# Kernel tuning notes

Measured on AMD Instinct MI355X. Metric: run time of the kernel, lower is better.

Reference implementation:

```python
import jax, jax.numpy as jnp
import numpy as np

B, S, D, H = 2, 2048, 1024, 16
HD = D // H  # head dim 64

def setup_inputs() -> dict:
    key = jax.random.key(0)
    k1, k2, k3 = jax.random.split(key, 3)
    x = jax.random.normal(k1, (B, S, D), dtype=jnp.float32)
    w_attn = jax.random.normal(k2, (D, 3 * D), dtype=jnp.float32) * (1.0 / np.sqrt(D))
    w_proj = jax.random.normal(k3, (D, D), dtype=jnp.float32) * (1.0 / np.sqrt(D))
    return {"x": x, "w_attn": w_attn, "w_proj": w_proj}

def reference(x, w_attn, w_proj):
    b, s, d = x.shape
    qkv = x @ w_attn                      # [b, s, 3d]
    q, k, v = jnp.split(qkv, 3, axis=-1)
    def heads(t):
        return t.reshape(b, s, H, HD).transpose(0, 2, 1, 3)  # [b, h, s, hd]
    q, k, v = heads(q), heads(k), heads(v)
    scale = 1.0 / np.sqrt(HD)
    att = jnp.einsum('bhqd,bhkd->bhqk', q, k) * scale        # [b, h, s, s]
    causal = jnp.tril(jnp.ones((s, s), dtype=bool))
    att = jnp.where(causal[None, None], att, -jnp.inf)
    att = jax.nn.softmax(att, axis=-1)
    y = jnp.einsum('bhqk,bhkd->bhqd', att, v)                # [b, h, s, hd]
    y = y.transpose(0, 2, 1, 3).reshape(b, s, d)
    return y @ w_proj
```

## Files before the change

### kernel.cpp

```cpp
#include <hip/hip_runtime.h>

#define B_  2
#define S_  2048
#define D_  1024
#define H_  16
#define HD_ 64
#define TD_ 3072

typedef __bf16 bf16x8 __attribute__((ext_vector_type(8)));
typedef float  f32x4  __attribute__((ext_vector_type(4)));
typedef float  f32x16 __attribute__((ext_vector_type(16)));

#define AS1 __attribute__((address_space(1)))
#define AS3 __attribute__((address_space(3)))

#define MASKVAL (-60000.0f)
#define MINITVAL (-30000.0f)

__device__ __forceinline__ unsigned short f2bf(float f) {
  return __builtin_bit_cast(unsigned short, (__bf16)f);
}

__device__ __forceinline__ unsigned int pkbf(float lo, float hi) {
  unsigned int r;
  asm("v_cvt_pk_bf16_f32 %0, %1, %2" : "=v"(r) : "v"(lo), "v"(hi));
  return r;
}

__device__ __forceinline__ void plswap(unsigned int& a, unsigned int& b) {
  asm volatile("v_permlane32_swap_b32 %0, %1" : "+v"(a), "+v"(b));
}

__device__ __forceinline__ float exp2a(float x) {
  return __builtin_amdgcn_exp2f(x);
}

__device__ __forceinline__ float xmax32(float x) {
  return fmaxf(x, __shfl_xor(x, 32, 64));
}
__device__ __forceinline__ float xadd32(float x) {
  return x + __shfl_xor(x, 32, 64);
}

__device__ __forceinline__ void gload16(const void* g, void* l) {
  __builtin_amdgcn_global_load_lds((const AS1 void*)g, (AS3 void*)l, 16, 0, 0);
}

__global__ __launch_bounds__(256) void k_convert_x(const float* __restrict__ x,
                                                   unsigned short* __restrict__ xb) {
  const int i = (blockIdx.x * 256 + threadIdx.x) * 4;
  float4 v = *(const float4*)(x + i);
  ushort4 o;
  o.x = f2bf(v.x); o.y = f2bf(v.y); o.z = f2bf(v.z); o.w = f2bf(v.w);
  *(ushort4*)(xb + i) = o;
}

__global__ __launch_bounds__(256) void k_prep_w(const float* __restrict__ wa,
                                                const float* __restrict__ wp,
                                                unsigned short* __restrict__ waT,
                                                unsigned short* __restrict__ wpT) {
  __shared__ __align__(16) unsigned short tile[64][72];
  const int t = threadIdx.x;
  const int bx = blockIdx.x;
  const float* w;
  unsigned short* wt;
  int C, c0;
  if (bx < 48) { w = wa; wt = waT; C = TD_; c0 = bx * 64; }
  else         { w = wp; wt = wpT; C = D_;  c0 = (bx - 48) * 64; }
  const int R = D_;
  const int r0 = blockIdx.y * 64;
  const int rr = t >> 2, cc = (t & 3) * 16;
  const float* src = w + (size_t)(r0 + rr) * C + c0 + cc;
#pragma unroll
  for (int j = 0; j < 16; j += 4) {
    float4 v = *(const float4*)(src + j);
    tile[rr][cc + j + 0] = f2bf(v.x);
    tile[rr][cc + j + 1] = f2bf(v.y);
    tile[rr][cc + j + 2] = f2bf(v.z);
    tile[rr][cc + j + 3] = f2bf(v.w);
  }
  __syncthreads();
  unsigned short* dst = wt + (size_t)(c0 + rr) * R + r0 + cc;
#pragma unroll
  for (int j = 0; j < 16; j += 2) {
    unsigned int pk = (unsigned int)tile[cc + j][rr] |
                      ((unsigned int)tile[cc + j + 1][rr] << 16);
    *(unsigned int*)(dst + j) = pk;
  }
}

__global__ __launch_bounds__(256) void k_gemm_qkv(const unsigned short* __restrict__ A,
                                                  const unsigned short* __restrict__ Bt,
                                                  unsigned short* __restrict__ qb,
                                                  unsigned short* __restrict__ kp,
                                                  unsigned short* __restrict__ vp) {
  __shared__ __align__(16) unsigned short ldsA[64 * 64];
  __shared__ __align__(16) unsigned short ldsB[128 * 64];
  const int K = D_;
  const int t = threadIdx.x;
  const int lane = t & 63;
  const int wid = t >> 6;
  const int wr = wid >> 1, wc = wid & 1;
  const int bx = blockIdx.x;
  const int bm = blockIdx.y * 64;
  const int bn = (((bx & 7) * 3) + (bx >> 3)) * 128;
  const int r = lane & 15, g = lane >> 4;

  f32x4 acc[2][4] = {};

  for (int kt = 0; kt < K; kt += 64) {
#pragma unroll
    for (int c = 0; c < 2; ++c) {
      const int idx = c * 256 + t;
      const int row = idx >> 3;
      const int col = ((idx & 7) ^ (row & 7)) * 8;
      gload16(A + (size_t)(bm + row) * K + kt + col, ldsA + idx * 8);
    }
#pragma unroll
    for (int c = 0; c < 4; ++c) {
      const int idx = c * 256 + t;
      const int row = idx >> 3;
      const int col = ((idx & 7) ^ (row & 7)) * 8;
      gload16(Bt + (size_t)(bn + row) * K + kt + col, ldsB + idx * 8);
    }
    asm volatile("s_waitcnt vmcnt(0)" ::: "memory");
    __syncthreads();
#pragma unroll
    for (int ks = 0; ks < 2; ++ks) {
      bf16x8 af[2], bfr[4];
#pragma unroll
      for (int m = 0; m < 2; ++m) {
        const int row = wr * 32 + m * 16 + r;
        const int slot = (ks * 4 + g) ^ (row & 7);
        af[m] = *(const bf16x8*)(ldsA + row * 64 + slot * 8);
      }
#pragma unroll
      for (int n = 0; n < 4; ++n) {
        const int row = wc * 64 + n * 16 + r;
        const int slot = (ks * 4 + g) ^ (row & 7);
        bfr[n] = *(const bf16x8*)(ldsB + row * 64 + slot * 8);
      }
#pragma unroll
      for (int m = 0; m < 2; ++m)
#pragma unroll
        for (int n = 0; n < 4; ++n)
          acc[m][n] = __builtin_amdgcn_mfma_f32_16x16x32_bf16(af[m], bfr[n],
                                                              acc[m][n], 0, 0, 0);
    }
    __syncthreads();
  }

  const int row0 = bm + wr * 32 + g * 4;
  const int col0 = bn + wc * 64 + r;
  const int region = bn >> 10;
  const int b = blockIdx.y >> 5;
  const int sbase = (bm & 2047) + wr * 32 + g * 4;

  if (region == 0) {
#pragma unroll
    for (int m = 0; m < 2; ++m)
#pragma unroll
      for (int n = 0; n < 4; ++n)
#pragma unroll
        for (int i = 0; i < 4; ++i)
          qb[(size_t)(row0 + m * 16 + i) * D_ + col0 + n * 16] = f2bf(acc[m][n][i]);
  } else if (region == 1) {
    const int h = ((bn - 1024) >> 6) + wc;
    unsigned short* kpb = kp + (size_t)(b * 16 + h) * 131072;
#pragma unroll
    for (int m = 0; m < 2; ++m) {
      const int s = sbase + m * 16;
      const int tau = s >> 5, l = s & 31;
#pragma unroll
      for (int n = 0; n < 4; ++n) {
        unsigned short* kq = kpb + tau * 2048 +
                             (n * 64 + (r >> 3) * 32 + l) * 8 + (r & 7);
        kq[0]  = f2bf(acc[m][n][0]);
        kq[8]  = f2bf(acc[m][n][1]);
        kq[16] = f2bf(acc[m][n][2]);
        kq[24] = f2bf(acc[m][n][3]);
      }
    }
  } else {
    const int h = ((bn - 2048) >> 6) + wc;
    unsigned short* vpb = vp + (size_t)(b * 16 + h) * 131072;
#pragma unroll
    for (int m = 0; m < 2; ++m) {
      const int s = sbase + m * 16;
      const int tau2 = s >> 6;
      const int T = (s >> 5) & 1, c16 = (s >> 4) & 1, hi8 = (s >> 3) & 1;
      const int u = s & 7;
#pragma unroll
      for (int n = 0; n < 4; ++n) {
        const int half = n >> 1;
        const int l = (n & 1) * 16 + r;
        const int tid = T * 256 + c16 * 128 + half * 64 + hi8 * 32 + l;
        unsigned long long pk2 =
            (unsigned long long)pkbf(acc[m][n][0], acc[m][n][1]) |
            ((unsigned long long)pkbf(acc[m][n][2], acc[m][n][3]) << 32);
        *(unsigned long long*)(vpb + tau2 * 4096 + tid * 8 + u) = pk2;
      }
    }
  }
}

__global__ __launch_bounds__(256) void k_gemm_bt64(const unsigned short* __restrict__ A,
                                                   const unsigned short* __restrict__ Bt,
                                                   float* __restrict__ C,
                                                   int Ndim, int K) {
  __shared__ __align__(16) unsigned short ldsA[64 * 64];
  __shared__ __align__(16) unsigned short ldsB[128 * 64];
  const int t = threadIdx.x;
  const int lane = t & 63;
  const int wid = t >> 6;
  const int wr = wid >> 1, wc = wid & 1;
  const int bm = blockIdx.y * 64, bn = blockIdx.x * 128;
  const int r = lane & 15, g = lane >> 4;

  f32x4 acc[2][4] = {};

  for (int kt = 0; kt < K; kt += 64) {
#pragma unroll
    for (int c = 0; c < 2; ++c) {
      const int idx = c * 256 + t;
      const int row = idx >> 3;
      const int col = ((idx & 7) ^ (row & 7)) * 8;
      gload16(A + (size_t)(bm + row) * K + kt + col, ldsA + idx * 8);
    }
#pragma unroll
    for (int c = 0; c < 4; ++c) {
      const int idx = c * 256 + t;
      const int row = idx >> 3;
      const int col = ((idx & 7) ^ (row & 7)) * 8;
      gload16(Bt + (size_t)(bn + row) * K + kt + col, ldsB + idx * 8);
    }
    asm volatile("s_waitcnt vmcnt(0)" ::: "memory");
    __syncthreads();
#pragma unroll
    for (int ks = 0; ks < 2; ++ks) {
      bf16x8 af[2], bfr[4];
#pragma unroll
      for (int m = 0; m < 2; ++m) {
        const int row = wr * 32 + m * 16 + r;
        const int slot = (ks * 4 + g) ^ (row & 7);
        af[m] = *(const bf16x8*)(ldsA + row * 64 + slot * 8);
      }
#pragma unroll
      for (int n = 0; n < 4; ++n) {
        const int row = wc * 64 + n * 16 + r;
        const int slot = (ks * 4 + g) ^ (row & 7);
        bfr[n] = *(const bf16x8*)(ldsB + row * 64 + slot * 8);
      }
#pragma unroll
      for (int m = 0; m < 2; ++m)
#pragma unroll
        for (int n = 0; n < 4; ++n)
          acc[m][n] = __builtin_amdgcn_mfma_f32_16x16x32_bf16(af[m], bfr[n],
                                                              acc[m][n], 0, 0, 0);
    }
    __syncthreads();
  }

  const int row0 = bm + wr * 32 + g * 4;
  const int col0 = bn + wc * 64 + r;
#pragma unroll
  for (int m = 0; m < 2; ++m)
#pragma unroll
    for (int n = 0; n < 4; ++n)
#pragma unroll
      for (int i = 0; i < 4; ++i)
        C[(size_t)(row0 + m * 16 + i) * Ndim + col0 + n * 16] = acc[m][n][i];
}

__global__ __launch_bounds__(256, 4) void k_attn(const unsigned short* __restrict__ qb,
                                                 const unsigned short* __restrict__ kp,
                                                 const unsigned short* __restrict__ vp,
                                                 unsigned short* __restrict__ y) {
  __shared__ __align__(16) float Om[2][64][32];
  __shared__ float Ml[2][2][32];
  const int t = threadIdx.x;
  const int lane = t & 63, w = t >> 6;
  const int l31 = lane & 31, hi = lane >> 5;
  const int pr = w & 1;
  const int parity = w >> 1;
  const int bh = blockIdx.x & 31;
  const int j = blockIdx.x >> 5;
  const int sj = pr ? (63 - j) : j;
  const int h = bh & 15, b = bh >> 4;
  const int qbase = 32 * sj;
  const int qq = qbase + l31;

  const float SC = 0.125f * 1.44269504f;

  bf16x8 qf[4];
  {
    const unsigned short* qp = qb + (size_t)(b * S_ + qbase + l31) * D_ + h * HD_;
#pragma unroll
    for (int c = 0; c < 4; ++c) {
      bf16x8 rl = *(const bf16x8*)(qp + c * 16 + hi * 8);
      union { unsigned int u[4]; bf16x8 v; } pl;
#pragma unroll
      for (int jx = 0; jx < 4; ++jx)
        pl.u[jx] = pkbf((float)rl[2 * jx] * SC, (float)rl[2 * jx + 1] * SC);
      qf[c] = pl.v;
    }
  }

  float mr = MINITVAL, lr = 0.f;
  f32x16 o0 = {}, o1 = {};

  const unsigned short* kpb = kp + (size_t)bh * 131072;
  const unsigned short* vpb = vp + (size_t)bh * 131072;

  const int tmax = (32 * sj + 31) >> 6;

  for (int kvt = parity; kvt <= tmax; kvt += 2) {
    const int kv0 = kvt << 6;
    bf16x8 kf[2][4];
#pragma unroll
    for (int T = 0; T < 2; ++T)
#pragma unroll
      for (int c = 0; c < 4; ++c)
        kf[T][c] = *(const bf16x8*)(kpb + (size_t)(kvt * 8 + T * 4 + c) * 512 +
                                    lane * 8);

    f32x16 s0 = {}, s1 = {};
    __builtin_amdgcn_s_setprio(1);
#pragma unroll
    for (int c = 0; c < 4; ++c) {
      s0 = __builtin_amdgcn_mfma_f32_32x32x16_bf16(kf[0][c], qf[c], s0, 0, 0, 0);
      s1 = __builtin_amdgcn_mfma_f32_32x32x16_bf16(kf[1][c], qf[c], s1, 0, 0, 0);
    }
    __builtin_amdgcn_s_setprio(0);

    float am[4] = {MASKVAL, MASKVAL, MASKVAL, MASKVAL};
    if (kv0 + 63 > qbase) {
#pragma unroll
      for (int rg = 0; rg < 16; ++rg) {
        const int kv = kv0 + (rg & 3) + 8 * (rg >> 2) + 4 * hi;
        float v0 = (kv <= qq) ? s0[rg] : MASKVAL; s0[rg] = v0;
        float v1 = (kv + 32 <= qq) ? s1[rg] : MASKVAL; s1[rg] = v1;
        am[rg & 3] = fmaxf(am[rg & 3], fmaxf(v0, v1));
      }
    } else {
#pragma unroll
      for (int rg = 0; rg < 16; ++rg)
        am[rg & 3] = fmaxf(am[rg & 3], fmaxf(s0[rg], s1[rg]));
    }
    const float pm = xmax32(fmaxf(fmaxf(am[0], am[1]), fmaxf(am[2], am[3])));

    const float nm = fmaxf(mr, pm);
    if (!__all(nm - mr <= 12.0f)) {
      const float cr = exp2a(mr - nm);
      mr = nm;
      lr *= cr;
#pragma unroll
      for (int rg = 0; rg < 16; ++rg) { o0[rg] *= cr; o1[rg] *= cr; }
    }

    float as[4] = {0.f, 0.f, 0.f, 0.f};
#pragma unroll
    for (int rg = 0; rg < 16; ++rg) {
      const float p0 = exp2a(s0[rg] - mr); s0[rg] = p0;
      const float p1 = exp2a(s1[rg] - mr); s1[rg] = p1;
      as[rg & 3] += p0 + p1;
    }
    lr += xadd32((as[0] + as[1]) + (as[2] + as[3]));

    const unsigned short* vpt = vpb + (size_t)kvt * 4096;
    __builtin_amdgcn_s_setprio(1);
#pragma unroll
    for (int T = 0; T < 2; ++T) {
      const f32x16& sT = T ? s1 : s0;
#pragma unroll
      for (int c = 0; c < 2; ++c) {
        unsigned int x0 = pkbf(sT[8 * c + 0], sT[8 * c + 1]);
        unsigned int x1 = pkbf(sT[8 * c + 2], sT[8 * c + 3]);
        unsigned int x2 = pkbf(sT[8 * c + 4], sT[8 * c + 5]);
        unsigned int x3 = pkbf(sT[8 * c + 6], sT[8 * c + 7]);
        plswap(x0, x2);
        plswap(x1, x3);
        union { unsigned int u[4]; bf16x8 v; } pb;
        pb.u[0] = x0; pb.u[1] = x1; pb.u[2] = x2; pb.u[3] = x3;
        const unsigned short* vb = vpt + (size_t)((T * 2 + c) * 2) * 512 + lane * 8;
        bf16x8 vf0 = *(const bf16x8*)(vb);
        bf16x8 vf1 = *(const bf16x8*)(vb + 512);
        o0 = __builtin_amdgcn_mfma_f32_32x32x16_bf16(vf0, pb.v, o0, 0, 0, 0);
        o1 = __builtin_amdgcn_mfma_f32_32x32x16_bf16(vf1, pb.v, o1, 0, 0, 0);
      }
    }
    __builtin_amdgcn_s_setprio(0);
  }

  __syncthreads();
  if (parity) {
#pragma unroll
    for (int tt = 0; tt < 2; ++tt) {
      const f32x16& o = tt ? o1 : o0;
#pragma unroll
      for (int rg = 0; rg < 16; ++rg) {
        const int row = tt * 32 + (rg & 3) + 8 * (rg >> 2) + 4 * hi;
        Om[pr][row][l31] = o[rg];
      }
    }
    if (!hi) {
      Ml[pr][0][l31] = mr;
      Ml[pr][1][l31] = lr;
    }
  }
  __syncthreads();
  if (!parity) {
    const float mo = Ml[pr][0][l31];
    const float lo2 = Ml[pr][1][l31];
    const float mm = fmaxf(mr, mo);
    const float ce = exp2a(mr - mm), co = exp2a(mo - mm);
    const float lt = lr * ce + lo2 * co;
    const float ic = ce / lt, io = co / lt;
    unsigned short* yp = y + (size_t)(b * S_ + qbase + l31) * D_ + h * HD_;
#pragma unroll
    for (int tt = 0; tt < 2; ++tt) {
      const f32x16& o = tt ? o1 : o0;
#pragma unroll
      for (int rg = 0; rg < 16; rg += 2) {
        const int row = tt * 32 + (rg & 3) + 8 * (rg >> 2) + 4 * hi;
        const float v0 = o[rg] * ic + Om[pr][row][l31] * io;
        const float v1 = o[rg + 1] * ic + Om[pr][row + 1][l31] * io;
        *(unsigned int*)(yp + row) = pkbf(v0, v1);
      }
    }
  }
}

extern "C" void kernel_launch(void* const* d_in, const int* in_sizes, int n_in,
                              void* d_out, int out_size, void* d_ws, size_t ws_size,
                              hipStream_t stream) {
  const float* x  = (const float*)d_in[0];
  const float* wa = (const float*)d_in[1];
  const float* wp = (const float*)d_in[2];
  float* out = (float*)d_out;

  char* ws = (char*)d_ws;
  unsigned short* xb  = (unsigned short*)(ws + 0);
  unsigned short* waT = (unsigned short*)(ws + 8388608);
  unsigned short* wpT = (unsigned short*)(ws + 14680064);
  unsigned short* qb  = (unsigned short*)(ws + 16777216);
  unsigned short* kp  = (unsigned short*)(ws + 25165824);
  unsigned short* vp  = (unsigned short*)(ws + 33554432);
  unsigned short* yb  = (unsigned short*)(ws + 41943040);

  k_convert_x<<<4096, 256, 0, stream>>>(x, xb);
  k_prep_w<<<dim3(64, 16), 256, 0, stream>>>(wa, wp, waT, wpT);
  k_gemm_qkv<<<dim3(24, 64), 256, 0, stream>>>(xb, waT, qb, kp, vp);
  k_attn<<<1024, 256, 0, stream>>>(qb, kp, vp, yb);
  k_gemm_bt64<<<dim3(8, 64), 256, 0, stream>>>(yb, wpT, out, D_, D_);
}
```

Baseline: 111.4 us.

## Double-buffer QKV GEMM LDS loads and merge input-prep kernels into one launch

The QKV GEMM now uses two LDS buffers, so the global-to-LDS loads for the next K tile are issued before the MFMAs run on the current tile. MFMA sections also get raised wave priority via s_setprio. Separately, the x conversion and weight transpose kernels are merged into one launch with a flattened grid, removing one kernel launch. Double buffering doubles LDS use per block (48KB), which may lower occupancy.

```diff
diff --git a/kernel.cpp b/kernel.cpp
--- a/kernel.cpp
+++ b/kernel.cpp
@@ -46,29 +46,33 @@
   __builtin_amdgcn_global_load_lds((const AS1 void*)g, (AS3 void*)l, 16, 0, 0);
 }
 
-__global__ __launch_bounds__(256) void k_convert_x(const float* __restrict__ x,
-                                                   unsigned short* __restrict__ xb) {
-  const int i = (blockIdx.x * 256 + threadIdx.x) * 4;
-  float4 v = *(const float4*)(x + i);
-  ushort4 o;
-  o.x = f2bf(v.x); o.y = f2bf(v.y); o.z = f2bf(v.z); o.w = f2bf(v.w);
-  *(ushort4*)(xb + i) = o;
-}
-
-__global__ __launch_bounds__(256) void k_prep_w(const float* __restrict__ wa,
-                                                const float* __restrict__ wp,
-                                                unsigned short* __restrict__ waT,
-                                                unsigned short* __restrict__ wpT) {
+__global__ __launch_bounds__(256) void k_prep(const float* __restrict__ x,
+                                              const float* __restrict__ wa,
+                                              const float* __restrict__ wp,
+                                              unsigned short* __restrict__ xb,
+                                              unsigned short* __restrict__ waT,
+                                              unsigned short* __restrict__ wpT) {
   __shared__ __align__(16) unsigned short tile[64][72];
   const int t = threadIdx.x;
-  const int bx = blockIdx.x;
+  const int bid = blockIdx.x;
+  if (bid < 4096) {
+    const int i = (bid * 256 + t) * 4;
+    float4 v = *(const float4*)(x + i);
+    ushort4 o;
+    o.x = f2bf(v.x); o.y = f2bf(v.y); o.z = f2bf(v.z); o.w = f2bf(v.w);
+    *(ushort4*)(xb + i) = o;
+    return;
+  }
+  const int idx = bid - 4096;
+  const int bx = idx & 63;
+  const int by = idx >> 6;
   const float* w;
   unsigned short* wt;
   int C, c0;
   if (bx < 48) { w = wa; wt = waT; C = TD_; c0 = bx * 64; }
   else         { w = wp; wt = wpT; C = D_;  c0 = (bx - 48) * 64; }
   const int R = D_;
-  const int r0 = blockIdx.y * 64;
+  const int r0 = by * 64;
   const int rr = t >> 2, cc = (t & 3) * 16;
   const float* src = w + (size_t)(r0 + rr) * C + c0 + cc;
 #pragma unroll
@@ -94,8 +98,8 @@
                                                   unsigned short* __restrict__ qb,
                                                   unsigned short* __restrict__ kp,
                                                   unsigned short* __restrict__ vp) {
-  __shared__ __align__(16) unsigned short ldsA[64 * 64];
-  __shared__ __align__(16) unsigned short ldsB[128 * 64];
+  __shared__ __align__(16) unsigned short ldsA[2][64 * 64];
+  __shared__ __align__(16) unsigned short ldsB[2][128 * 64];
   const int K = D_;
   const int t = threadIdx.x;
   const int lane = t & 63;
@@ -108,23 +112,32 @@
 
   f32x4 acc[2][4] = {};
 
-  for (int kt = 0; kt < K; kt += 64) {
+  auto stage = [&](int buf, int kt) {
 #pragma unroll
     for (int c = 0; c < 2; ++c) {
       const int idx = c * 256 + t;
       const int row = idx >> 3;
       const int col = ((idx & 7) ^ (row & 7)) * 8;
-      gload16(A + (size_t)(bm + row) * K + kt + col, ldsA + idx * 8);
+      gload16(A + (size_t)(bm + row) * K + kt + col, &ldsA[buf][idx * 8]);
     }
 #pragma unroll
     for (int c = 0; c < 4; ++c) {
       const int idx = c * 256 + t;
       const int row = idx >> 3;
       const int col = ((idx & 7) ^ (row & 7)) * 8;
-      gload16(Bt + (size_t)(bn + row) * K + kt + col, ldsB + idx * 8);
-    }
-    asm volatile("s_waitcnt vmcnt(0)" ::: "memory");
-    __syncthreads();
+      gload16(Bt + (size_t)(bn + row) * K + kt + col, &ldsB[buf][idx * 8]);
+    }
+  };
+
+  stage(0, 0);
+  asm volatile("s_waitcnt vmcnt(0)" ::: "memory");
+  __syncthreads();
+
+  int cur = 0;
+  for (int kt = 0; kt < K; kt += 64) {
+    if (kt + 64 < K) stage(cur ^ 1, kt + 64);
+
+    __builtin_amdgcn_s_setprio(1);
 #pragma unroll
     for (int ks = 0; ks < 2; ++ks) {
       bf16x8 af[2], bfr[4];
@@ -132,13 +145,13 @@
       for (int m = 0; m < 2; ++m) {
         const int row = wr * 32 + m * 16 + r;
         const int slot = (ks * 4 + g) ^ (row & 7);
-        af[m] = *(const bf16x8*)(ldsA + row * 64 + slot * 8);
+        af[m] = *(const bf16x8*)(&ldsA[cur][row * 64 + slot * 8]);
       }
 #pragma unroll
       for (int n = 0; n < 4; ++n) {
         const int row = wc * 64 + n * 16 + r;
         const int slot = (ks * 4 + g) ^ (row & 7);
-        bfr[n] = *(const bf16x8*)(ldsB + row * 64 + slot * 8);
+        bfr[n] = *(const bf16x8*)(&ldsB[cur][row * 64 + slot * 8]);
       }
 #pragma unroll
       for (int m = 0; m < 2; ++m)
@@ -147,7 +160,11 @@
           acc[m][n] = __builtin_amdgcn_mfma_f32_16x16x32_bf16(af[m], bfr[n],
                                                               acc[m][n], 0, 0, 0);
     }
+    __builtin_amdgcn_s_setprio(0);
+
+    asm volatile("s_waitcnt vmcnt(0)" ::: "memory");
     __syncthreads();
+    cur ^= 1;
   }
 
   const int row0 = bm + wr * 32 + g * 4;
@@ -448,8 +465,7 @@
   unsigned short* vp  = (unsigned short*)(ws + 33554432);
   unsigned short* yb  = (unsigned short*)(ws + 41943040);
 
-  k_convert_x<<<4096, 256, 0, stream>>>(x, xb);
-  k_prep_w<<<dim3(64, 16), 256, 0, stream>>>(wa, wp, waT, wpT);
+  k_prep<<<5120, 256, 0, stream>>>(x, wa, wp, xb, waT, wpT);
   k_gemm_qkv<<<dim3(24, 64), 256, 0, stream>>>(xb, waT, qb, kp, vp);
   k_attn<<<1024, 256, 0, stream>>>(qb, kp, vp, yb);
   k_gemm_bt64<<<dim3(8, 64), 256, 0, stream>>>(yb, wpT, out, D_, D_);
```

After: 106.0 us. -4.8%, faster.
